# Optimization experiments

Measured on AMD Instinct MI355X. Metric: run time of the kernel, lower is better.

The kernel has to match this reference:

```python
import jax, jax.numpy as jnp
import numpy as np
import math

B, T, O = 4, 1024, 128
D, H, L, V = 512, 8, 6, 128
M, EH = 100000, 4
EHD = D // EH
HD = D // H
TK = O + 2 * T
PAD_ID = 0
NGRAM = 4

def _primes():
    ps = []
    base = 131
    for h in range(EH):
        x = base + h * 1009
        row = []
        for _ in range(NGRAM):
            row.append(x % (2 ** 32))
            x = x * 31 + 1
        ps.append(row)
    return jnp.array(ps, dtype=jnp.uint32)

PRIMES = _primes()

def rmsnorm(x, scale, eps=1e-6):
    return x / jnp.sqrt(jnp.mean(jnp.square(x), axis=-1, keepdims=True) + eps) * scale

def precompute_freqs_cis(dim, max_len, theta=10000.0):
    freqs = 1.0 / theta ** (jnp.arange(0, dim, 2, dtype=jnp.float32) / dim)
    t = jnp.arange(max_len, dtype=jnp.float32)
    return jnp.exp(1j * jnp.outer(t, freqs))[None, :, None, :]  # (1, max_len, 1, dim/2)

def apply_rope(x, f):
    b, t, h, d = x.shape
    xc = jax.lax.complex(x[..., 0::2], x[..., 1::2])
    xr = xc * f
    return jnp.stack([xr.real, xr.imag], axis=-1).reshape(b, t, h, d)

def setup_inputs() -> dict:
    key = jax.random.key(0)
    ks = jax.random.split(key, 16)
    rn = lambda k, shp, s=0.02: jax.random.normal(k, shp, jnp.float32) * s
    logit = lambda p: float(np.log(p / (1.0 - p)))
    return {
        'tokens_w': jax.random.randint(ks[0], (B, T), 0, V, dtype=jnp.int32),
        'mem_ids': jax.random.randint(ks[1], (B, O), 0, V, dtype=jnp.int32),
        'mem_emb': jax.random.normal(ks[2], (B, O, D), jnp.float32),
        'ssum': jax.random.normal(ks[3], (B, D), jnp.float32),
        'embed_table': rn(ks[4], (V, D)),
        'engram_table': rn(ks[5], (M, EH, EHD)),
        'engram_gate': jnp.full((EH, EHD), -2.0, jnp.float32),
        'engram_scale': jnp.ones(D, jnp.float32),
        'mem_W': rn(ks[6], (D, D)), 'mem_b': jnp.zeros(D, jnp.float32),
        'mem_scale': jnp.ones(D, jnp.float32),
        'alpha_gate': jnp.full((D,), logit(0.1), jnp.float32),
        'ssum_W': rn(ks[7], (D, D)),
        'ln1': jnp.ones((L, D), jnp.float32),
        'qW': rn(ks[8], (L, D, D)), 'qb': jnp.zeros((L, D), jnp.float32),
        'kW': rn(ks[9], (L, D, D)), 'kb': jnp.zeros((L, D), jnp.float32),
        'vW': rn(ks[10], (L, D, D)), 'vb': jnp.zeros((L, D), jnp.float32),
        'oW': rn(ks[11], (L, D, D)), 'ob': jnp.zeros((L, D), jnp.float32),
        'ln2': jnp.ones((L, D), jnp.float32),
        'w_in': rn(ks[12], (L, D, 8 * D)),
        'w_out': rn(ks[13], (L, 4 * D, D)),
        'final_scale': jnp.ones(D, jnp.float32),
    }

def _forward(tokens_w, mem_ids, mem_emb, ssum, embed_table, engram_table, engram_gate,
             engram_scale, mem_W, mem_b, mem_scale, alpha_gate, ssum_W,
             ln1, qW, qb, kW, kb, vW, vb, oW, ob, ln2, w_in, w_out, final_scale):
    # token embedding
    x = embed_table[tokens_w]  # (B,T,D)
    # multi-head engram: rolling n-gram hash lookup
    cur = jnp.where(tokens_w == PAD_ID, 0, tokens_w).astype(jnp.uint32)
    prev = jnp.where(mem_ids == PAD_ID, 0, mem_ids).astype(jnp.uint32)
    full = jnp.concatenate([prev, cur], axis=1)  # (B, O+T)
    hs = jnp.zeros((B, T, EH), jnp.uint32)
    for i in range(NGRAM):
        chunk = full[:, O - i: O + T - i]
        hs = hs + chunk[:, :, None] * PRIMES[None, None, :, i]
    idx = (hs % jnp.uint32(M)).astype(jnp.int32)  # (B,T,EH)
    retr = engram_table[idx, jnp.arange(EH)[None, None, :], :]  # (B,T,EH,EHD)
    eng = (retr * jax.nn.sigmoid(engram_gate)[None, None]).reshape(B, T, D)
    eng = rmsnorm(eng, engram_scale)
    # memory adapter + state-sum injection
    mem_p = rmsnorm(mem_emb @ mem_W + mem_b, mem_scale)
    alpha = jax.nn.sigmoid(alpha_gate)
    x = x + (ssum @ ssum_W)[:, None, :] * alpha[None, None, :]
    kv_seq = jnp.concatenate([mem_p, eng, x], axis=1)  # (B, TK, D)
    # masks: mem fully visible, engram + current causal; pad invalid keys
    tril = jnp.tril(jnp.ones((T, T), bool))
    full_mask = jnp.concatenate([jnp.ones((T, O), bool), tril, tril], axis=1)
    valid_curr = tokens_w != PAD_ID
    valid_k = jnp.concatenate([jnp.ones((B, O), bool), valid_curr, valid_curr], axis=1)
    mask = full_mask[None, None] & valid_k[:, None, None, :]  # (B,1,T,TK)
    freqs = precompute_freqs_cis(HD, TK + 32)
    fq, fk = freqs[:, :T], freqs[:, :TK]
    scale = 1.0 / math.sqrt(HD)

    def block(cx, p):
        ln1_, qW_, qb_, kW_, kb_, vW_, vb_, oW_, ob_, ln2_, wi_, wo_ = p
        nx = rmsnorm(cx, ln1_)
        q = (nx @ qW_ + qb_).reshape(B, T, H, HD)
        k = (kv_seq @ kW_ + kb_).reshape(B, TK, H, HD)
        v = (kv_seq @ vW_ + vb_).reshape(B, TK, H, HD)
        q = apply_rope(q, fq)
        k = apply_rope(k, fk)
        scores = jnp.einsum('bqhd,bkhd->bhqk', q, k) * scale
        scores = jnp.where(mask, scores, -1e9)
        probs = jax.nn.softmax(scores, axis=-1)
        o = jnp.einsum('bhqk,bkhd->bqhd', probs, v).reshape(B, T, D)
        cx = cx + o @ oW_ + ob_
        n2 = rmsnorm(cx, ln2_)
        gate, val = jnp.split(n2 @ wi_, 2, axis=-1)
        cx = cx + (jax.nn.silu(gate) * val) @ wo_
        return cx, None

    curr_x, _ = jax.lax.scan(block, x, (ln1, qW, qb, kW, kb, vW, vb, oW, ob, ln2, w_in, w_out))
    return rmsnorm(curr_x, final_scale)

def reference(tokens_w, mem_ids, mem_emb, ssum, embed_table, engram_table, engram_gate,
              engram_scale, mem_W, mem_b, mem_scale, alpha_gate, ssum_W,
              ln1, qW, qb, kW, kb, vW, vb, oW, ob, ln2, w_in, w_out, final_scale):
    return _forward(tokens_w, mem_ids, mem_emb, ssum, embed_table, engram_table, engram_gate,
                    engram_scale, mem_W, mem_b, mem_scale, alpha_gate, ssum_W,
                    ln1, qW, qb, kW, kb, vW, vb, oW, ob, ln2, w_in, w_out, final_scale)
```

## Files before the change

kernel.cpp:

```cpp
#include <hip/hip_runtime.h>
#include <hip/hip_bf16.h>
#include <math.h>

#define B_ 4
#define T_ 1024
#define O_ 128
#define D_ 512
#define H_ 8
#define L_ 6
#define TK_ 2176
#define MM_ 100000
#define EH_ 4
#define EHD_ 128
#define HD_ 64

typedef float f32x4 __attribute__((ext_vector_type(4)));
typedef short bf16x8 __attribute__((ext_vector_type(8)));
typedef unsigned short u16;

__device__ __constant__ unsigned int PRIMES_[4][4] = {
  {131u,  4062u,  125923u, 3903614u},
  {1140u, 35341u, 1095572u, 33962733u},
  {2149u, 66620u, 2065221u, 64021852u},
  {3158u, 97899u, 3034870u, 94080971u},
};

__device__ __forceinline__ float wave_sum_f(float v) {
  #pragma unroll
  for (int off = 32; off; off >>= 1) v += __shfl_xor(v, off);
  return v;
}

__device__ __forceinline__ short f2bf(float f) {
  unsigned int u = __float_as_uint(f);
  unsigned int r = (u + 0x7fffu + ((u >> 16) & 1u)) >> 16;
  return (short)r;
}

__device__ __forceinline__ void gload16(const void* g, void* l) {
  __builtin_amdgcn_global_load_lds((const __attribute__((address_space(1))) void*)g,
                                   (__attribute__((address_space(3))) void*)l, 16, 0, 0);
}

__global__ __launch_bounds__(64) void rope_table_k(float* __restrict__ rc,
                                                   float* __restrict__ rs) {
  int i = blockIdx.x * 64 + threadIdx.x;
  int t = i >> 5, j = i & 31;
  float freq = __powf(10000.0f, -(float)j / 32.0f);
  float ang = (float)t * freq;
  rc[i] = cosf(ang);
  rs[i] = sinf(ang);
}

__global__ __launch_bounds__(256) void ssum_proj_k(const float* __restrict__ ssum,
                                                   const float* __restrict__ sW,
                                                   float* __restrict__ ssp) {
  int col = blockIdx.x * 256 + threadIdx.x;
  int b = blockIdx.y;
  float acc = 0.f;
  for (int d = 0; d < D_; ++d) acc += ssum[b * D_ + d] * sW[(size_t)d * D_ + col];
  ssp[b * D_ + col] = acc;
}

__global__ __launch_bounds__(256) void sgemm_k(const float* __restrict__ A,
                                               const float* __restrict__ W,
                                               const float* __restrict__ bias,
                                               float* __restrict__ C,
                                               int M, int N, int K) {
  __shared__ float As[16][68];
  __shared__ float Bs[16][68];
  int tid = threadIdx.x;
  int row0 = blockIdx.y * 64;
  int col0 = blockIdx.x * 64;
  int tx = tid & 15, ty = tid >> 4;
  int am = tid >> 2, ak = (tid & 3) * 4;
  int bk = tid >> 4, bc = (tid & 15) * 4;
  float acc[4][4] = {};
  for (int k0 = 0; k0 < K; k0 += 16) {
    float4 av = *reinterpret_cast<const float4*>(&A[(size_t)(row0 + am) * K + k0 + ak]);
    As[ak + 0][am] = av.x; As[ak + 1][am] = av.y; As[ak + 2][am] = av.z; As[ak + 3][am] = av.w;
    float4 bv = *reinterpret_cast<const float4*>(&W[(size_t)(k0 + bk) * N + col0 + bc]);
    *reinterpret_cast<float4*>(&Bs[bk][bc]) = bv;
    __syncthreads();
    #pragma unroll
    for (int kk = 0; kk < 16; ++kk) {
      float4 a4 = *reinterpret_cast<const float4*>(&As[kk][ty * 4]);
      float4 b4 = *reinterpret_cast<const float4*>(&Bs[kk][tx * 4]);
      float a[4] = {a4.x, a4.y, a4.z, a4.w};
      float b[4] = {b4.x, b4.y, b4.z, b4.w};
      #pragma unroll
      for (int i = 0; i < 4; ++i)
        #pragma unroll
        for (int j = 0; j < 4; ++j) acc[i][j] += a[i] * b[j];
    }
    __syncthreads();
  }
  int cbase = col0 + tx * 4;
  float4 b4 = *reinterpret_cast<const float4*>(&bias[cbase]);
  float bb[4] = {b4.x, b4.y, b4.z, b4.w};
  #pragma unroll
  for (int i = 0; i < 4; ++i) {
    int row = row0 + ty * 4 + i;
    *reinterpret_cast<float4*>(&C[(size_t)row * N + cbase]) =
        make_float4(acc[i][0] + bb[0], acc[i][1] + bb[1], acc[i][2] + bb[2], acc[i][3] + bb[3]);
  }
}

__device__ __forceinline__ void wconv_tile(const float* __restrict__ W, u16* __restrict__ wT,
                                           int K, int N) {
  __shared__ float s[64][65];
  int n0 = blockIdx.x * 64, k0 = blockIdx.y * 64;
  int tid = threadIdx.x;
  int kr = tid >> 4, nc = (tid & 15) * 4;
  #pragma unroll
  for (int kk = 0; kk < 4; ++kk) {
    float4 f = *reinterpret_cast<const float4*>(&W[(size_t)(k0 + kr + kk * 16) * N + n0 + nc]);
    s[kr + kk * 16][nc + 0] = f.x; s[kr + kk * 16][nc + 1] = f.y;
    s[kr + kk * 16][nc + 2] = f.z; s[kr + kk * 16][nc + 3] = f.w;
  }
  __syncthreads();
  int nr = tid >> 4, kc = (tid & 15) * 4;
  #pragma unroll
  for (int nn = 0; nn < 4; ++nn) {
    int n = nr + nn * 16;
    ushort4 o;
    o.x = (u16)f2bf(s[kc + 0][n]); o.y = (u16)f2bf(s[kc + 1][n]);
    o.z = (u16)f2bf(s[kc + 2][n]); o.w = (u16)f2bf(s[kc + 3][n]);
    *reinterpret_cast<ushort4*>(&wT[(size_t)(n0 + n) * K + k0 + kc]) = o;
  }
}

__global__ __launch_bounds__(256) void wconv_qkvo_k(const float* __restrict__ qW,
                                                    const float* __restrict__ kW,
                                                    const float* __restrict__ vW,
                                                    const float* __restrict__ oW,
                                                    u16* __restrict__ dst) {
  int z = blockIdx.z;
  int l = z >> 2, which = z & 3;
  const float* src = which == 0 ? qW : which == 1 ? kW : which == 2 ? vW : oW;
  wconv_tile(src + (size_t)l * D_ * D_, dst + (size_t)z * D_ * D_, D_, D_);
}

__global__ __launch_bounds__(256) void wconv_win_k(const float* __restrict__ w_in,
                                                   u16* __restrict__ dst) {
  int l = blockIdx.z;
  wconv_tile(w_in + (size_t)l * 512 * 4096, dst + (size_t)l * 4096 * 512, 512, 4096);
}

__global__ __launch_bounds__(256) void wconv_wout_k(const float* __restrict__ w_out,
                                                    u16* __restrict__ dst) {
  int l = blockIdx.z;
  wconv_tile(w_out + (size_t)l * 2048 * 512, dst + (size_t)l * 512 * 2048, 2048, 512);
}

template<int EPI, int MI>
__global__ __launch_bounds__(256) void gemm_bf16_k(const u16* __restrict__ A,
                                                   const u16* __restrict__ Bt,
                                                   const float* __restrict__ bias,
                                                   void* __restrict__ Cout,
                                                   int M, int N, int K, int posmod,
                                                   const float* __restrict__ rc,
                                                   const float* __restrict__ rs) {
  __shared__ __align__(16) u16 As[2][MI * 32 * 32];
  __shared__ __align__(16) u16 Bs[2][128 * 32];
  int tid = threadIdx.x;
  int w = tid >> 6, lane = tid & 63;
  int lr = lane & 15, lg = lane >> 4;
  int row0 = blockIdx.y * (MI * 32), col0 = blockIdx.x * 128;
  int wr = w >> 1, wc = w & 1;
  f32x4 acc[MI][4] = {};

  int srow = lane >> 2;
  int skel = (lane & 3) * 8;

  auto stage = [&](int buf, int k0) {
    if constexpr (MI == 4) {
      #pragma unroll
      for (int ci = 0; ci < 2; ++ci) {
        int c = w * 2 + ci;
        gload16(A + (size_t)(row0 + c * 16 + srow) * K + k0 + skel, &As[buf][c * 512]);
      }
    } else {
      gload16(A + (size_t)(row0 + w * 16 + srow) * K + k0 + skel, &As[buf][w * 512]);
    }
    #pragma unroll
    for (int ci = 0; ci < 2; ++ci) {
      int c = w * 2 + ci;
      gload16(Bt + (size_t)(col0 + c * 16 + srow) * K + k0 + skel, &Bs[buf][c * 512]);
    }
  };

  stage(0, 0);
  __syncthreads();
  int nk = K >> 5;
  int buf = 0;
  for (int t = 0; t < nk; ++t) {
    if (t + 1 < nk) stage(buf ^ 1, (t + 1) * 32);
    bf16x8 af[MI], bfr[4];
    #pragma unroll
    for (int i = 0; i < MI; ++i)
      af[i] = *reinterpret_cast<const bf16x8*>(
          &As[buf][(wr * (16 * MI) + i * 16 + lr) * 32 + lg * 8]);
    #pragma unroll
    for (int j = 0; j < 4; ++j)
      bfr[j] = *reinterpret_cast<const bf16x8*>(&Bs[buf][(wc * 64 + j * 16 + lr) * 32 + lg * 8]);
    #pragma unroll
    for (int i = 0; i < MI; ++i)
      #pragma unroll
      for (int j = 0; j < 4; ++j)
        acc[i][j] = __builtin_amdgcn_mfma_f32_16x16x32_bf16(af[i], bfr[j], acc[i][j], 0, 0, 0);
    __syncthreads();
    buf ^= 1;
  }

  #pragma unroll
  for (int j = 0; j < 4; ++j) {
    int col = col0 + wc * 64 + j * 16 + lr;
    float bs = bias ? bias[col] : 0.f;
    #pragma unroll
    for (int i = 0; i < MI; ++i) {
      #pragma unroll
      for (int r = 0; r < 4; ++r) {
        int row = row0 + wr * (16 * MI) + i * 16 + lg * 4 + r;
        float v = acc[i][j][r] + bs;
        if (EPI == 1) {
          int pos = row % posmod;
          int d = col & 63;
          float c = rc[(size_t)pos * 32 + (d >> 1)];
          float s = rs[(size_t)pos * 32 + (d >> 1)];
          float partner = __shfl_xor(v, 1);
          v = (d & 1) ? (partner * s + v * c) : (v * c - partner * s);
        }
        if (EPI == 2) {
          float* Cf = (float*)Cout;
          Cf[(size_t)row * N + col] += v;
        } else {
          u16* Cb = (u16*)Cout;
          Cb[(size_t)row * N + col] = (u16)f2bf(v);
        }
      }
    }
  }
}

__global__ __launch_bounds__(256) void kv_gemm_k(const u16* __restrict__ A,
                                                 const u16* __restrict__ wqkvoT,
                                                 const float* __restrict__ kbias_all,
                                                 const float* __restrict__ vbias_all,
                                                 u16* __restrict__ kb_base,
                                                 u16* __restrict__ vb_base,
                                                 const float* __restrict__ rc,
                                                 const float* __restrict__ rs,
                                                 int l0, size_t ostride) {
  __shared__ __align__(16) u16 As[2][128 * 32];
  __shared__ __align__(16) u16 Bk[2][64 * 32];
  __shared__ __align__(16) u16 Bv[2][64 * 32];
  const int K = 512, N = 512;
  int l = l0 + blockIdx.z;
  const u16* wkT = wqkvoT + ((size_t)l * 4 + 1) * (D_ * D_);
  const u16* wvT = wqkvoT + ((size_t)l * 4 + 2) * (D_ * D_);
  const float* kbias = kbias_all + l * D_;
  const float* vbias = vbias_all + l * D_;
  u16* kb = kb_base + (size_t)blockIdx.z * ostride;
  u16* vb = vb_base + (size_t)blockIdx.z * ostride;
  int tid = threadIdx.x;
  int w = tid >> 6, lane = tid & 63;
  int lr = lane & 15, lg = lane >> 4;
  int row0 = blockIdx.y * 128, col0 = blockIdx.x * 64;
  int wr = w >> 1, wc = w & 1;
  f32x4 ak_[4][2] = {};
  f32x4 av_[4][2] = {};

  int srow = lane >> 2;
  int skel = (lane & 3) * 8;

  auto stage = [&](int buf, int k0) {
    #pragma unroll
    for (int ci = 0; ci < 2; ++ci) {
      int c = w * 2 + ci;
      gload16(A + (size_t)(row0 + c * 16 + srow) * K + k0 + skel, &As[buf][c * 512]);
    }
    gload16(wkT + (size_t)(col0 + w * 16 + srow) * K + k0 + skel, &Bk[buf][w * 512]);
    gload16(wvT + (size_t)(col0 + w * 16 + srow) * K + k0 + skel, &Bv[buf][w * 512]);
  };

  stage(0, 0);
  __syncthreads();
  int buf = 0;
  for (int t = 0; t < 16; ++t) {
    if (t + 1 < 16) stage(buf ^ 1, (t + 1) * 32);
    bf16x8 af[4], bk[2], bv[2];
    #pragma unroll
    for (int i = 0; i < 4; ++i)
      af[i] = *reinterpret_cast<const bf16x8*>(&As[buf][(wr * 64 + i * 16 + lr) * 32 + lg * 8]);
    #pragma unroll
    for (int j = 0; j < 2; ++j) {
      bk[j] = *reinterpret_cast<const bf16x8*>(&Bk[buf][(wc * 32 + j * 16 + lr) * 32 + lg * 8]);
      bv[j] = *reinterpret_cast<const bf16x8*>(&Bv[buf][(wc * 32 + j * 16 + lr) * 32 + lg * 8]);
    }
    #pragma unroll
    for (int i = 0; i < 4; ++i)
      #pragma unroll
      for (int j = 0; j < 2; ++j) {
        ak_[i][j] = __builtin_amdgcn_mfma_f32_16x16x32_bf16(af[i], bk[j], ak_[i][j], 0, 0, 0);
        av_[i][j] = __builtin_amdgcn_mfma_f32_16x16x32_bf16(af[i], bv[j], av_[i][j], 0, 0, 0);
      }
    __syncthreads();
    buf ^= 1;
  }

  #pragma unroll
  for (int j = 0; j < 2; ++j) {
    int col = col0 + wc * 32 + j * 16 + lr;
    float kbs = kbias[col], vbs = vbias[col];
    int d = col & 63;
    #pragma unroll
    for (int i = 0; i < 4; ++i) {
      #pragma unroll
      for (int r = 0; r < 4; ++r) {
        int row = row0 + wr * 64 + i * 16 + lg * 4 + r;
        int pos = row % TK_;
        float vk = ak_[i][j][r] + kbs;
        float c = rc[(size_t)pos * 32 + (d >> 1)];
        float s = rs[(size_t)pos * 32 + (d >> 1)];
        float partner = __shfl_xor(vk, 1);
        vk = (d & 1) ? (partner * s + vk * c) : (vk * c - partner * s);
        kb[(size_t)row * N + col] = (u16)f2bf(vk);
        vb[(size_t)row * N + col] = (u16)f2bf(av_[i][j][r] + vbs);
      }
    }
  }
}

__global__ __launch_bounds__(256) void mlp_in_mfma_k(const u16* __restrict__ A,
                                                     const u16* __restrict__ wiT,
                                                     u16* __restrict__ Hout) {
  __shared__ __align__(16) u16 As[2][128 * 32];
  __shared__ __align__(16) u16 Bg[2][64 * 32];
  __shared__ __align__(16) u16 Bv[2][64 * 32];
  int tid = threadIdx.x;
  int w = tid >> 6, lane = tid & 63;
  int lr = lane & 15, lg = lane >> 4;
  int hc0 = blockIdx.x * 64, row0 = blockIdx.y * 128;
  int wr = w >> 1, wc = w & 1;
  f32x4 ag[4][2] = {};
  f32x4 av[4][2] = {};
  const int K = 512;

  int srow = lane >> 2;
  int skel = (lane & 3) * 8;

  auto stage = [&](int buf, int k0) {
    #pragma unroll
    for (int ci = 0; ci < 2; ++ci) {
      int c = w * 2 + ci;
      gload16(A + (size_t)(row0 + c * 16 + srow) * K + k0 + skel, &As[buf][c * 512]);
    }
    gload16(wiT + (size_t)(hc0 + w * 16 + srow) * K + k0 + skel, &Bg[buf][w * 512]);
    gload16(wiT + (size_t)(2048 + hc0 + w * 16 + srow) * K + k0 + skel, &Bv[buf][w * 512]);
  };

  stage(0, 0);
  __syncthreads();
  int buf = 0;
  for (int t = 0; t < 16; ++t) {
    if (t + 1 < 16) stage(buf ^ 1, (t + 1) * 32);
    bf16x8 af[4], bg[2], bv[2];
    #pragma unroll
    for (int i = 0; i < 4; ++i)
      af[i] = *reinterpret_cast<const bf16x8*>(&As[buf][(wr * 64 + i * 16 + lr) * 32 + lg * 8]);
    #pragma unroll
    for (int j = 0; j < 2; ++j) {
      bg[j] = *reinterpret_cast<const bf16x8*>(&Bg[buf][(wc * 32 + j * 16 + lr) * 32 + lg * 8]);
      bv[j] = *reinterpret_cast<const bf16x8*>(&Bv[buf][(wc * 32 + j * 16 + lr) * 32 + lg * 8]);
    }
    #pragma unroll
    for (int i = 0; i < 4; ++i)
      #pragma unroll
      for (int j = 0; j < 2; ++j) {
        ag[i][j] = __builtin_amdgcn_mfma_f32_16x16x32_bf16(af[i], bg[j], ag[i][j], 0, 0, 0);
        av[i][j] = __builtin_amdgcn_mfma_f32_16x16x32_bf16(af[i], bv[j], av[i][j], 0, 0, 0);
      }
    __syncthreads();
    buf ^= 1;
  }

  #pragma unroll
  for (int j = 0; j < 2; ++j) {
    int col = hc0 + wc * 32 + j * 16 + lr;
    #pragma unroll
    for (int i = 0; i < 4; ++i) {
      #pragma unroll
      for (int r = 0; r < 4; ++r) {
        int row = row0 + wr * 64 + i * 16 + lg * 4 + r;
        float g = ag[i][j][r];
        float sg = g / (1.f + __expf(-g));
        Hout[(size_t)row * 2048 + col] = (u16)f2bf(sg * av[i][j][r]);
      }
    }
  }
}

template<int OUTBF>
__global__ __launch_bounds__(128) void rmsnorm_k(const float* __restrict__ in,
                                                 const float* __restrict__ scale,
                                                 void* __restrict__ out) {
  int row = blockIdx.x;
  int tid = threadIdx.x;
  float4 v = *reinterpret_cast<const float4*>(&in[(size_t)row * D_ + tid * 4]);
  float ss = v.x * v.x + v.y * v.y + v.z * v.z + v.w * v.w;
  ss = wave_sum_f(ss);
  __shared__ float red[2];
  if ((tid & 63) == 0) red[tid >> 6] = ss;
  __syncthreads();
  ss = red[0] + red[1];
  float inv = 1.0f / sqrtf(ss / (float)D_ + 1e-6f);
  float4 sc = *reinterpret_cast<const float4*>(&scale[tid * 4]);
  float o0 = v.x * inv * sc.x, o1 = v.y * inv * sc.y, o2 = v.z * inv * sc.z, o3 = v.w * inv * sc.w;
  if (OUTBF) {
    ushort4 o;
    o.x = (u16)f2bf(o0); o.y = (u16)f2bf(o1); o.z = (u16)f2bf(o2); o.w = (u16)f2bf(o3);
    *reinterpret_cast<ushort4*>((u16*)out + (size_t)row * D_ + tid * 4) = o;
  } else {
    *reinterpret_cast<float4*>((float*)out + (size_t)row * D_ + tid * 4) =
        make_float4(o0, o1, o2, o3);
  }
}

__global__ __launch_bounds__(128) void memnorm_k(const float* __restrict__ tmp,
                                                 const float* __restrict__ scale,
                                                 u16* __restrict__ kv) {
  int o = blockIdx.x, b = blockIdx.y;
  int tid = threadIdx.x;
  float4 v = *reinterpret_cast<const float4*>(&tmp[(size_t)(b * O_ + o) * D_ + tid * 4]);
  float ss = v.x * v.x + v.y * v.y + v.z * v.z + v.w * v.w;
  ss = wave_sum_f(ss);
  __shared__ float red[2];
  if ((tid & 63) == 0) red[tid >> 6] = ss;
  __syncthreads();
  ss = red[0] + red[1];
  float inv = 1.0f / sqrtf(ss / (float)D_ + 1e-6f);
  float4 sc = *reinterpret_cast<const float4*>(&scale[tid * 4]);
  ushort4 oo;
  oo.x = (u16)f2bf(v.x * inv * sc.x); oo.y = (u16)f2bf(v.y * inv * sc.y);
  oo.z = (u16)f2bf(v.z * inv * sc.z); oo.w = (u16)f2bf(v.w * inv * sc.w);
  *reinterpret_cast<ushort4*>(&kv[(size_t)(b * TK_ + o) * D_ + tid * 4]) = oo;
}

__global__ __launch_bounds__(128) void engram_k(const int* __restrict__ tokens,
                                                const int* __restrict__ mem_ids,
                                                const float* __restrict__ etab,
                                                const float* __restrict__ egate,
                                                const float* __restrict__ escale,
                                                u16* __restrict__ kv) {
  int t = blockIdx.x, b = blockIdx.y;
  int tid = threadIdx.x;
  unsigned int toks[4];
  #pragma unroll
  for (int i = 0; i < 4; ++i) {
    int idx = t - i;
    toks[i] = (idx >= 0) ? (unsigned int)tokens[b * T_ + idx]
                         : (unsigned int)mem_ids[b * O_ + O_ + idx];
  }
  int c = tid * 4;
  int h = c >> 7;
  int e = c & 127;
  unsigned int hs = 0;
  #pragma unroll
  for (int i = 0; i < 4; ++i) hs += toks[i] * PRIMES_[h][i];
  int idxh = (int)(hs % (unsigned int)MM_);
  float4 r = *reinterpret_cast<const float4*>(&etab[((size_t)idxh * EH_ + h) * EHD_ + e]);
  float4 g = *reinterpret_cast<const float4*>(&egate[h * EHD_ + e]);
  float4 val;
  val.x = r.x / (1.f + __expf(-g.x));
  val.y = r.y / (1.f + __expf(-g.y));
  val.z = r.z / (1.f + __expf(-g.z));
  val.w = r.w / (1.f + __expf(-g.w));
  float ss = val.x * val.x + val.y * val.y + val.z * val.z + val.w * val.w;
  ss = wave_sum_f(ss);
  __shared__ float red[2];
  if ((tid & 63) == 0) red[tid >> 6] = ss;
  __syncthreads();
  ss = red[0] + red[1];
  float inv = 1.0f / sqrtf(ss / (float)D_ + 1e-6f);
  float4 sc = *reinterpret_cast<const float4*>(&escale[c]);
  ushort4 oo;
  oo.x = (u16)f2bf(val.x * inv * sc.x); oo.y = (u16)f2bf(val.y * inv * sc.y);
  oo.z = (u16)f2bf(val.z * inv * sc.z); oo.w = (u16)f2bf(val.w * inv * sc.w);
  *reinterpret_cast<ushort4*>(&kv[(size_t)(b * TK_ + O_ + t) * D_ + c]) = oo;
}

__global__ __launch_bounds__(128) void embed_k(const int* __restrict__ tokens,
                                               const float* __restrict__ etab,
                                               const float* __restrict__ ssp,
                                               const float* __restrict__ alpha_g,
                                               float* __restrict__ cx,
                                               u16* __restrict__ kv) {
  int t = blockIdx.x, b = blockIdx.y;
  int tid = threadIdx.x;
  int c = tid * 4;
  int tok = tokens[b * T_ + t];
  float4 e = *reinterpret_cast<const float4*>(&etab[(size_t)tok * D_ + c]);
  float4 sp = *reinterpret_cast<const float4*>(&ssp[b * D_ + c]);
  float4 ag = *reinterpret_cast<const float4*>(&alpha_g[c]);
  float4 x;
  x.x = e.x + sp.x / (1.f + __expf(-ag.x));
  x.y = e.y + sp.y / (1.f + __expf(-ag.y));
  x.z = e.z + sp.z / (1.f + __expf(-ag.z));
  x.w = e.w + sp.w / (1.f + __expf(-ag.w));
  *reinterpret_cast<float4*>(&cx[(size_t)(b * T_ + t) * D_ + c]) = x;
  ushort4 oo;
  oo.x = (u16)f2bf(x.x); oo.y = (u16)f2bf(x.y);
  oo.z = (u16)f2bf(x.z); oo.w = (u16)f2bf(x.w);
  *reinterpret_cast<ushort4*>(&kv[(size_t)(b * TK_ + O_ + T_ + t) * D_ + c]) = oo;
}

#define KIDX8(r, c) (((r) << 6) + ((c) ^ (((r) & 7) << 3)))
#define KIDX4(r, c) (((r) << 6) + ((c) ^ (((r) & 15) << 2)))
#define PIDX(q, o) (((q) << 5) + ((o) ^ (((q) & 7) << 2)))

__global__ __launch_bounds__(512) void attn_mfma_k(const u16* __restrict__ qb,
                                                   const u16* __restrict__ kb,
                                                   const u16* __restrict__ vb,
                                                   const int* __restrict__ tokens,
                                                   u16* __restrict__ ob) {
  __shared__ __align__(16) short ks[2][64 * 64];
  __shared__ __align__(16) short vst[2][64 * 64];
  __shared__ __align__(16) unsigned int pbuf[8][16 * 32];
  __shared__ unsigned char vtok[T_];

  int fid = blockIdx.x;
  int h = fid & 7;
  int s = fid >> 3;
  int pair = s & 7;
  int b = s >> 3;
  int bxA = pair, bxB = 15 - pair;

  int tid = threadIdx.x;
  int w = tid >> 6, lane = tid & 63;
  int lr = lane & 15;
  int lg = lane >> 4;
  int myBx = (w < 4) ? bxA : bxB;
  int qw0 = myBx * 64 + (w & 3) * 16;
  int tq = qw0 + lr;

  for (int i = tid; i < T_; i += 512) vtok[i] = (tokens[b * T_ + i] != 0);

  bf16x8 aq[2];
  {
    const u16* qp = &qb[((size_t)(b * T_) + tq) * D_ + h * 64];
    aq[0] = *reinterpret_cast<const bf16x8*>(qp + lg * 8);
    aq[1] = *reinterpret_cast<const bf16x8*>(qp + 32 + lg * 8);
  }

  float m_ = -1e30f, lsum = 0.f;
  f32x4 od[4];
  #pragma unroll
  for (int dt = 0; dt < 4; ++dt) od[dt] = (f32x4){0.f, 0.f, 0.f, 0.f};

  int sr = tid >> 3;
  int sc = (tid & 7) * 8;
  int vr2 = (tid >> 4) * 2;
  int vc = (tid & 15) * 4;

  int nt = 2 + 2 * (bxB + 1);
  auto tile_pos = [&](int i, int& pos0, int& base, bool& masked, bool& part) {
    if (i < 2) { pos0 = i * 64; base = 0; masked = false; part = true; }
    else if (i < 3 + bxB) {
      int t = i - 2;
      pos0 = O_ + t * 64; base = O_; masked = true; part = (t <= myBx);
    } else {
      int t = i - (3 + bxB);
      pos0 = O_ + T_ + t * 64; base = O_ + T_; masked = true; part = (t <= myBx);
    }
  };

  bf16x8 pk0;
  short4 pv0, pv1;

  auto load_regs = [&](int pos0) {
    const u16* kg = &kb[((size_t)(b * TK_) + pos0 + sr) * D_ + h * 64 + sc];
    pk0 = *reinterpret_cast<const bf16x8*>(kg);
    const u16* vg = &vb[((size_t)(b * TK_) + pos0 + vr2) * D_ + h * 64 + vc];
    pv0 = *reinterpret_cast<const short4*>(vg);
    pv1 = *reinterpret_cast<const short4*>(vg + D_);
  };

  auto write_lds = [&](int buf) {
    *reinterpret_cast<bf16x8*>(&ks[buf][KIDX8(sr, sc)]) = pk0;
    unsigned int t0 = (unsigned int)(u16)pv0.x | ((unsigned int)(u16)pv1.x << 16);
    unsigned int t1 = (unsigned int)(u16)pv0.y | ((unsigned int)(u16)pv1.y << 16);
    unsigned int t2 = (unsigned int)(u16)pv0.z | ((unsigned int)(u16)pv1.z << 16);
    unsigned int t3 = (unsigned int)(u16)pv0.w | ((unsigned int)(u16)pv1.w << 16);
    *reinterpret_cast<unsigned int*>(&vst[buf][KIDX4(vc + 0, vr2)]) = t0;
    *reinterpret_cast<unsigned int*>(&vst[buf][KIDX4(vc + 1, vr2)]) = t1;
    *reinterpret_cast<unsigned int*>(&vst[buf][KIDX4(vc + 2, vr2)]) = t2;
    *reinterpret_cast<unsigned int*>(&vst[buf][KIDX4(vc + 3, vr2)]) = t3;
  };

  unsigned int* pw = (unsigned int*)pbuf[w];

  auto compute = [&](int buf, int pos0, int base, bool masked) {
    float sv[4][4];
    __builtin_amdgcn_s_setprio(1);
    #pragma unroll
    for (int kt = 0; kt < 4; ++kt) {
      bf16x8 ka0 = *reinterpret_cast<const bf16x8*>(&ks[buf][KIDX8(kt * 16 + lr, lg * 8)]);
      bf16x8 ka1 = *reinterpret_cast<const bf16x8*>(&ks[buf][KIDX8(kt * 16 + lr, 32 + lg * 8)]);
      f32x4 sf = (f32x4){0.f, 0.f, 0.f, 0.f};
      sf = __builtin_amdgcn_mfma_f32_16x16x32_bf16(ka0, aq[0], sf, 0, 0, 0);
      sf = __builtin_amdgcn_mfma_f32_16x16x32_bf16(ka1, aq[1], sf, 0, 0, 0);
      #pragma unroll
      for (int r = 0; r < 4; ++r) sv[kt][r] = sf[r];
    }
    __builtin_amdgcn_s_setprio(0);
    if (masked) {
      #pragma unroll
      for (int kt = 0; kt < 4; ++kt) {
        #pragma unroll
        for (int r = 0; r < 4; ++r) {
          int tk = pos0 + kt * 16 + lg * 4 + r - base;
          bool valid = (vtok[tk] != 0) && (tk <= tq);
          sv[kt][r] = valid ? sv[kt][r] * 0.125f : -1e30f;
        }
      }
    } else {
      #pragma unroll
      for (int kt = 0; kt < 4; ++kt)
        #pragma unroll
        for (int r = 0; r < 4; ++r) sv[kt][r] *= 0.125f;
    }
    float pmax = sv[0][0];
    #pragma unroll
    for (int kt = 0; kt < 4; ++kt)
      #pragma unroll
      for (int r = 0; r < 4; ++r) pmax = fmaxf(pmax, sv[kt][r]);
    pmax = fmaxf(pmax, __shfl_xor(pmax, 16));
    pmax = fmaxf(pmax, __shfl_xor(pmax, 32));
    float mnew = fmaxf(m_, pmax);
    float al = __expf(m_ - mnew);
    m_ = mnew;
    float psum = 0.f;
    #pragma unroll
    for (int kt = 0; kt < 4; ++kt)
      #pragma unroll
      for (int r = 0; r < 4; ++r) {
        float pe = __expf(sv[kt][r] - mnew);
        sv[kt][r] = pe;
        psum += pe;
      }
    psum += __shfl_xor(psum, 16);
    psum += __shfl_xor(psum, 32);
    lsum = lsum * al + psum;
    #pragma unroll
    for (int dt = 0; dt < 4; ++dt) {
      f32x4 o = od[dt];
      o[0] *= al; o[1] *= al; o[2] *= al; o[3] *= al;
      od[dt] = o;
    }
    #pragma unroll
    for (int kt = 0; kt < 4; ++kt) {
      uint2 wp;
      asm("v_cvt_pk_bf16_f32 %0, %1, %2" : "=v"(wp.x) : "v"(sv[kt][0]), "v"(sv[kt][1]));
      asm("v_cvt_pk_bf16_f32 %0, %1, %2" : "=v"(wp.y) : "v"(sv[kt][2]), "v"(sv[kt][3]));
      *reinterpret_cast<uint2*>(&pw[PIDX(lr, kt * 8 + lg * 2)]) = wp;
    }
    bf16x8 pf0 = *reinterpret_cast<const bf16x8*>(&pw[PIDX(lr, lg * 4)]);
    bf16x8 pf1 = *reinterpret_cast<const bf16x8*>(&pw[PIDX(lr, 16 + lg * 4)]);
    __builtin_amdgcn_s_setprio(1);
    #pragma unroll
    for (int dt = 0; dt < 4; ++dt) {
      short4 lo0 = *reinterpret_cast<const short4*>(&vst[buf][KIDX4(dt * 16 + lr, lg * 8)]);
      short4 hi0 = *reinterpret_cast<const short4*>(&vst[buf][KIDX4(dt * 16 + lr, lg * 8 + 4)]);
      short4 lo1 = *reinterpret_cast<const short4*>(&vst[buf][KIDX4(dt * 16 + lr, 32 + lg * 8)]);
      short4 hi1 = *reinterpret_cast<const short4*>(&vst[buf][KIDX4(dt * 16 + lr, 36 + lg * 8)]);
      bf16x8 va0 = {lo0.x, lo0.y, lo0.z, lo0.w, hi0.x, hi0.y, hi0.z, hi0.w};
      bf16x8 va1 = {lo1.x, lo1.y, lo1.z, lo1.w, hi1.x, hi1.y, hi1.z, hi1.w};
      od[dt] = __builtin_amdgcn_mfma_f32_16x16x32_bf16(va0, pf0, od[dt], 0, 0, 0);
      od[dt] = __builtin_amdgcn_mfma_f32_16x16x32_bf16(va1, pf1, od[dt], 0, 0, 0);
    }
    __builtin_amdgcn_s_setprio(0);
  };

  {
    int pos0, base; bool masked, part;
    tile_pos(0, pos0, base, masked, part);
    load_regs(pos0);
  }
  for (int i = 0; i < nt; ++i) {
    write_lds(i & 1);
    __syncthreads();
    int pos0, base; bool masked, part;
    tile_pos(i, pos0, base, masked, part);
    if (i + 1 < nt) {
      int npos, nbase; bool nmask, npart;
      tile_pos(i + 1, npos, nbase, nmask, npart);
      load_regs(npos);
    }
    if (part) compute(i & 1, pos0, base, masked);
  }

  float inv = 1.0f / lsum;
  #pragma unroll
  for (int dt = 0; dt < 4; ++dt) {
    ushort4 o4;
    o4.x = (u16)f2bf(od[dt][0] * inv);
    o4.y = (u16)f2bf(od[dt][1] * inv);
    o4.z = (u16)f2bf(od[dt][2] * inv);
    o4.w = (u16)f2bf(od[dt][3] * inv);
    *reinterpret_cast<ushort4*>(
        &ob[((size_t)(b * T_) + tq) * D_ + h * 64 + dt * 16 + lg * 4]) = o4;
  }
}

extern "C" void kernel_launch(void* const* d_in, const int* in_sizes, int n_in,
                              void* d_out, int out_size, void* d_ws, size_t ws_size,
                              hipStream_t stream) {
  (void)in_sizes; (void)n_in; (void)out_size;
  const int* tokens = (const int*)d_in[0];
  const int* mem_ids = (const int*)d_in[1];
  const float* mem_emb = (const float*)d_in[2];
  const float* ssum = (const float*)d_in[3];
  const float* embed = (const float*)d_in[4];
  const float* engram_t = (const float*)d_in[5];
  const float* engram_g = (const float*)d_in[6];
  const float* engram_s = (const float*)d_in[7];
  const float* mem_W = (const float*)d_in[8];
  const float* mem_b = (const float*)d_in[9];
  const float* mem_s = (const float*)d_in[10];
  const float* alpha_g = (const float*)d_in[11];
  const float* ssum_W = (const float*)d_in[12];
  const float* ln1 = (const float*)d_in[13];
  const float* qW = (const float*)d_in[14];
  const float* qbias = (const float*)d_in[15];
  const float* kW = (const float*)d_in[16];
  const float* kbias = (const float*)d_in[17];
  const float* vW = (const float*)d_in[18];
  const float* vbias = (const float*)d_in[19];
  const float* oW = (const float*)d_in[20];
  const float* obias = (const float*)d_in[21];
  const float* ln2 = (const float*)d_in[22];
  const float* w_in = (const float*)d_in[23];
  const float* w_out = (const float*)d_in[24];
  const float* final_s = (const float*)d_in[25];

  const size_t KVSZ = (size_t)B_ * TK_ * D_;
  size_t need = (KVSZ * 2 * 2 * L_) + 120u * 1024 * 1024;
  bool batched = ws_size >= need;

  char* p = (char*)d_ws;
  auto alloc = [&](size_t bytes) { char* r = p; p += (bytes + 255) & ~(size_t)255; return r; };
  u16* kv_b   = (u16*)alloc(KVSZ * 2);
  float* cx   = (float*)alloc((size_t)B_ * T_ * D_ * 4);
  u16* nx_b   = (u16*)alloc((size_t)B_ * T_ * D_ * 2);
  u16* qb_b   = (u16*)alloc((size_t)B_ * T_ * D_ * 2);
  int nkv = batched ? L_ : 1;
  u16* kb_all = (u16*)alloc(KVSZ * 2 * nkv);
  u16* vb_all = (u16*)alloc(KVSZ * 2 * nkv);
  u16* hb;
  if (batched) hb = (u16*)alloc((size_t)B_ * T_ * 2048 * 2);
  else hb = kb_all;
  u16* wqkvoT = (u16*)alloc((size_t)L_ * 4 * D_ * D_ * 2);
  u16* wiT    = (u16*)alloc((size_t)L_ * 4096 * 512 * 2);
  u16* woutT  = (u16*)alloc((size_t)L_ * 512 * 2048 * 2);
  float* ssp  = (float*)alloc((size_t)B_ * D_ * 4);
  float* rc   = (float*)alloc((size_t)TK_ * 32 * 4);
  float* rs   = (float*)alloc((size_t)TK_ * 32 * 4);
  float* mem_tmp = (float*)qb_b;
  u16* ob_b = nx_b;

  rope_table_k<<<TK_ * 32 / 64, 64, 0, stream>>>(rc, rs);
  wconv_qkvo_k<<<dim3(8, 8, L_ * 4), 256, 0, stream>>>(qW, kW, vW, oW, wqkvoT);
  wconv_win_k<<<dim3(64, 8, L_), 256, 0, stream>>>(w_in, wiT);
  wconv_wout_k<<<dim3(8, 32, L_), 256, 0, stream>>>(w_out, woutT);
  ssum_proj_k<<<dim3(2, B_), 256, 0, stream>>>(ssum, ssum_W, ssp);
  sgemm_k<<<dim3(8, 8), 256, 0, stream>>>(mem_emb, mem_W, mem_b, mem_tmp, B_ * O_, D_, D_);
  memnorm_k<<<dim3(O_, B_), 128, 0, stream>>>(mem_tmp, mem_s, kv_b);
  engram_k<<<dim3(T_, B_), 128, 0, stream>>>(tokens, mem_ids, engram_t, engram_g, engram_s, kv_b);
  embed_k<<<dim3(T_, B_), 128, 0, stream>>>(tokens, embed, ssp, alpha_g, cx, kv_b);

  if (batched) {
    kv_gemm_k<<<dim3(8, 68, L_), 256, 0, stream>>>(kv_b, wqkvoT, kbias, vbias,
                                                   kb_all, vb_all, rc, rs, 0, KVSZ);
  }

  const size_t WSZ = (size_t)D_ * D_;
  for (int l = 0; l < L_; ++l) {
    const u16* wqT = wqkvoT + ((size_t)l * 4 + 0) * WSZ;
    const u16* woT = wqkvoT + ((size_t)l * 4 + 3) * WSZ;
    const u16* wil = wiT + (size_t)l * 4096 * 512;
    const u16* wol = woutT + (size_t)l * 512 * 2048;
    u16* kb_l = batched ? kb_all + (size_t)l * KVSZ : kb_all;
    u16* vb_l = batched ? vb_all + (size_t)l * KVSZ : vb_all;

    rmsnorm_k<1><<<B_ * T_, 128, 0, stream>>>(cx, ln1 + l * D_, nx_b);
    gemm_bf16_k<1, 2><<<dim3(4, 64), 256, 0, stream>>>(nx_b, wqT, qbias + l * D_, qb_b,
                                                       B_ * T_, D_, D_, T_, rc, rs);
    if (!batched) {
      kv_gemm_k<<<dim3(8, 68, 1), 256, 0, stream>>>(kv_b, wqkvoT, kbias, vbias,
                                                    kb_l, vb_l, rc, rs, l, 0);
    }
    attn_mfma_k<<<dim3(256), 512, 0, stream>>>(qb_b, kb_l, vb_l, tokens, ob_b);
    gemm_bf16_k<2, 2><<<dim3(4, 64), 256, 0, stream>>>(ob_b, woT, obias + l * D_, cx,
                                                       B_ * T_, D_, D_, 0, nullptr, nullptr);
    rmsnorm_k<1><<<B_ * T_, 128, 0, stream>>>(cx, ln2 + l * D_, nx_b);
    mlp_in_mfma_k<<<dim3(32, 32), 256, 0, stream>>>(nx_b, wil, hb);
    gemm_bf16_k<2, 2><<<dim3(4, 64), 256, 0, stream>>>(hb, wol, nullptr, cx,
                                                       B_ * T_, D_, 2048, 0, nullptr, nullptr);
  }
  rmsnorm_k<0><<<B_ * T_, 128, 0, stream>>>(cx, final_s, d_out);
}
```

Measured before the change: 1.156 ms.

## Shrink per-layer GEMM tiles to 64x64 and stage KV epilogue stores through LDS

Replaces the templated 64x128 GEMM with a 64x64-tile kernel for the Q, output-projection and MLP-out GEMMs, doubling the grid from 256 to 512 blocks to fill more compute units on the 4096x512 outputs. Separately, the KV GEMM epilogue now writes K and V results into shared memory and then emits 16-byte vectorized global stores, replacing scattered 2-byte stores. Smaller tiles lower per-block operand reuse and raise global traffic per FLOP. The staging path adds extra barriers.

```diff
diff --git a/kernel.cpp b/kernel.cpp
--- a/kernel.cpp
+++ b/kernel.cpp
@@ -153,41 +153,29 @@
   wconv_tile(w_out + (size_t)l * 2048 * 512, dst + (size_t)l * 512 * 2048, 2048, 512);
 }
 
-template<int EPI, int MI>
-__global__ __launch_bounds__(256) void gemm_bf16_k(const u16* __restrict__ A,
-                                                   const u16* __restrict__ Bt,
-                                                   const float* __restrict__ bias,
-                                                   void* __restrict__ Cout,
-                                                   int M, int N, int K, int posmod,
-                                                   const float* __restrict__ rc,
-                                                   const float* __restrict__ rs) {
-  __shared__ __align__(16) u16 As[2][MI * 32 * 32];
-  __shared__ __align__(16) u16 Bs[2][128 * 32];
+template<int EPI>
+__global__ __launch_bounds__(256) void gemm_sm_k(const u16* __restrict__ A,
+                                                 const u16* __restrict__ Bt,
+                                                 const float* __restrict__ bias,
+                                                 void* __restrict__ Cout,
+                                                 int M, int N, int K, int posmod,
+                                                 const float* __restrict__ rc,
+                                                 const float* __restrict__ rs) {
+  __shared__ __align__(16) u16 As[2][64 * 32];
+  __shared__ __align__(16) u16 Bs[2][64 * 32];
   int tid = threadIdx.x;
   int w = tid >> 6, lane = tid & 63;
   int lr = lane & 15, lg = lane >> 4;
-  int row0 = blockIdx.y * (MI * 32), col0 = blockIdx.x * 128;
+  int row0 = blockIdx.y * 64, col0 = blockIdx.x * 64;
   int wr = w >> 1, wc = w & 1;
-  f32x4 acc[MI][4] = {};
-
-  int srow = lane >> 2;
-  int skel = (lane & 3) * 8;
+  f32x4 acc[2][2] = {};
+
+  int srow = tid >> 2;
+  int skel = (tid & 3) * 8;
 
   auto stage = [&](int buf, int k0) {
-    if constexpr (MI == 4) {
-      #pragma unroll
-      for (int ci = 0; ci < 2; ++ci) {
-        int c = w * 2 + ci;
-        gload16(A + (size_t)(row0 + c * 16 + srow) * K + k0 + skel, &As[buf][c * 512]);
-      }
-    } else {
-      gload16(A + (size_t)(row0 + w * 16 + srow) * K + k0 + skel, &As[buf][w * 512]);
-    }
-    #pragma unroll
-    for (int ci = 0; ci < 2; ++ci) {
-      int c = w * 2 + ci;
-      gload16(Bt + (size_t)(col0 + c * 16 + srow) * K + k0 + skel, &Bs[buf][c * 512]);
-    }
+    gload16(A + (size_t)(row0 + srow) * K + k0 + skel, &As[buf][srow * 32 + skel]);
+    gload16(Bt + (size_t)(col0 + srow) * K + k0 + skel, &Bs[buf][srow * 32 + skel]);
   };
 
   stage(0, 0);
@@ -196,32 +184,31 @@
   int buf = 0;
   for (int t = 0; t < nk; ++t) {
     if (t + 1 < nk) stage(buf ^ 1, (t + 1) * 32);
-    bf16x8 af[MI], bfr[4];
-    #pragma unroll
-    for (int i = 0; i < MI; ++i)
-      af[i] = *reinterpret_cast<const bf16x8*>(
-          &As[buf][(wr * (16 * MI) + i * 16 + lr) * 32 + lg * 8]);
-    #pragma unroll
-    for (int j = 0; j < 4; ++j)
-      bfr[j] = *reinterpret_cast<const bf16x8*>(&Bs[buf][(wc * 64 + j * 16 + lr) * 32 + lg * 8]);
-    #pragma unroll
-    for (int i = 0; i < MI; ++i)
-      #pragma unroll
-      for (int j = 0; j < 4; ++j)
-        acc[i][j] = __builtin_amdgcn_mfma_f32_16x16x32_bf16(af[i], bfr[j], acc[i][j], 0, 0, 0);
+    bf16x8 af[2], bf[2];
+    #pragma unroll
+    for (int i = 0; i < 2; ++i)
+      af[i] = *reinterpret_cast<const bf16x8*>(&As[buf][(wr * 32 + i * 16 + lr) * 32 + lg * 8]);
+    #pragma unroll
+    for (int j = 0; j < 2; ++j)
+      bf[j] = *reinterpret_cast<const bf16x8*>(&Bs[buf][(wc * 32 + j * 16 + lr) * 32 + lg * 8]);
+    #pragma unroll
+    for (int i = 0; i < 2; ++i)
+      #pragma unroll
+      for (int j = 0; j < 2; ++j)
+        acc[i][j] = __builtin_amdgcn_mfma_f32_16x16x32_bf16(af[i], bf[j], acc[i][j], 0, 0, 0);
     __syncthreads();
     buf ^= 1;
   }
 
   #pragma unroll
-  for (int j = 0; j < 4; ++j) {
-    int col = col0 + wc * 64 + j * 16 + lr;
+  for (int j = 0; j < 2; ++j) {
+    int col = col0 + wc * 32 + j * 16 + lr;
     float bs = bias ? bias[col] : 0.f;
     #pragma unroll
-    for (int i = 0; i < MI; ++i) {
+    for (int i = 0; i < 2; ++i) {
       #pragma unroll
       for (int r = 0; r < 4; ++r) {
-        int row = row0 + wr * (16 * MI) + i * 16 + lg * 4 + r;
+        int row = row0 + wr * 32 + i * 16 + lg * 4 + r;
         float v = acc[i][j][r] + bs;
         if (EPI == 1) {
           int pos = row % posmod;
@@ -309,26 +296,43 @@
     buf ^= 1;
   }
 
-  #pragma unroll
-  for (int j = 0; j < 2; ++j) {
-    int col = col0 + wc * 32 + j * 16 + lr;
-    float kbs = kbias[col], vbs = vbias[col];
-    int d = col & 63;
-    #pragma unroll
-    for (int i = 0; i < 4; ++i) {
-      #pragma unroll
-      for (int r = 0; r < 4; ++r) {
-        int row = row0 + wr * 64 + i * 16 + lg * 4 + r;
-        int pos = row % TK_;
-        float vk = ak_[i][j][r] + kbs;
-        float c = rc[(size_t)pos * 32 + (d >> 1)];
-        float s = rs[(size_t)pos * 32 + (d >> 1)];
-        float partner = __shfl_xor(vk, 1);
-        vk = (d & 1) ? (partner * s + vk * c) : (vk * c - partner * s);
-        kb[(size_t)row * N + col] = (u16)f2bf(vk);
-        vb[(size_t)row * N + col] = (u16)f2bf(av_[i][j][r] + vbs);
+  u16* stg = &As[0][0];
+  __syncthreads();
+  #pragma unroll
+  for (int pass = 0; pass < 2; ++pass) {
+    #pragma unroll
+    for (int j = 0; j < 2; ++j) {
+      int lcol = wc * 32 + j * 16 + lr;
+      int gcol = col0 + lcol;
+      float bs = pass ? vbias[gcol] : kbias[gcol];
+      int d = gcol & 63;
+      #pragma unroll
+      for (int i = 0; i < 4; ++i) {
+        #pragma unroll
+        for (int r = 0; r < 4; ++r) {
+          int lrow = wr * 64 + i * 16 + lg * 4 + r;
+          float v = (pass ? av_[i][j][r] : ak_[i][j][r]) + bs;
+          if (!pass) {
+            int pos = (row0 + lrow) % TK_;
+            float c = rc[(size_t)pos * 32 + (d >> 1)];
+            float s = rs[(size_t)pos * 32 + (d >> 1)];
+            float partner = __shfl_xor(v, 1);
+            v = (d & 1) ? (partner * s + v * c) : (v * c - partner * s);
+          }
+          stg[lrow * 64 + lcol] = (u16)f2bf(v);
+        }
       }
     }
+    __syncthreads();
+    {
+      int trow = tid >> 1, tc0 = (tid & 1) * 32;
+      u16* dst = (pass ? vb : kb) + (size_t)(row0 + trow) * N + col0 + tc0;
+      const u16* src = &stg[trow * 64 + tc0];
+      #pragma unroll
+      for (int c = 0; c < 4; ++c)
+        *reinterpret_cast<bf16x8*>(dst + c * 8) = *reinterpret_cast<const bf16x8*>(src + c * 8);
+    }
+    __syncthreads();
   }
 }
 
@@ -794,19 +798,19 @@
     u16* vb_l = batched ? vb_all + (size_t)l * KVSZ : vb_all;
 
     rmsnorm_k<1><<<B_ * T_, 128, 0, stream>>>(cx, ln1 + l * D_, nx_b);
-    gemm_bf16_k<1, 2><<<dim3(4, 64), 256, 0, stream>>>(nx_b, wqT, qbias + l * D_, qb_b,
-                                                       B_ * T_, D_, D_, T_, rc, rs);
+    gemm_sm_k<1><<<dim3(8, 64), 256, 0, stream>>>(nx_b, wqT, qbias + l * D_, qb_b,
+                                                  B_ * T_, D_, D_, T_, rc, rs);
     if (!batched) {
       kv_gemm_k<<<dim3(8, 68, 1), 256, 0, stream>>>(kv_b, wqkvoT, kbias, vbias,
                                                     kb_l, vb_l, rc, rs, l, 0);
     }
     attn_mfma_k<<<dim3(256), 512, 0, stream>>>(qb_b, kb_l, vb_l, tokens, ob_b);
-    gemm_bf16_k<2, 2><<<dim3(4, 64), 256, 0, stream>>>(ob_b, woT, obias + l * D_, cx,
-                                                       B_ * T_, D_, D_, 0, nullptr, nullptr);
+    gemm_sm_k<2><<<dim3(8, 64), 256, 0, stream>>>(ob_b, woT, obias + l * D_, cx,
+                                                  B_ * T_, D_, D_, 0, nullptr, nullptr);
     rmsnorm_k<1><<<B_ * T_, 128, 0, stream>>>(cx, ln2 + l * D_, nx_b);
     mlp_in_mfma_k<<<dim3(32, 32), 256, 0, stream>>>(nx_b, wil, hb);
-    gemm_bf16_k<2, 2><<<dim3(4, 64), 256, 0, stream>>>(hb, wol, nullptr, cx,
-                                                       B_ * T_, D_, 2048, 0, nullptr, nullptr);
+    gemm_sm_k<2><<<dim3(8, 64), 256, 0, stream>>>(hb, wol, nullptr, cx,
+                                                  B_ * T_, D_, 2048, 0, nullptr, nullptr);
   }
   rmsnorm_k<0><<<B_ * T_, 128, 0, stream>>>(cx, final_s, d_out);
 }
```

Measured after the change: 1.088 ms. 5.9% less time.
